# Performance work log

Measured on AMD Instinct MI355X. Metric: run time of the kernel, lower is better.

Reference implementation:

```python
import jax, jax.numpy as jnp
from jax import lax
import numpy as np
import math

B, H, W = 4, 64, 64
D_MODEL, D_STATE, D_CONV, EXPAND, K = 96, 16, 3, 2, 4
D_INNER = EXPAND * D_MODEL          # 192
DT_RANK = math.ceil(D_MODEL / 16)   # 6


def setup_inputs() -> dict:
    key = jax.random.key(0)
    ks = jax.random.split(key, 12)
    s = 0.02
    rgb = jax.random.normal(ks[0], (B, H, W, D_MODEL), jnp.float32)
    t = jax.random.normal(ks[1], (B, H, W, D_MODEL), jnp.float32)
    in_proj1_w = jax.random.normal(ks[2], (2 * D_INNER, D_MODEL), jnp.float32) * s
    in_proj2_w = jax.random.normal(ks[3], (2 * D_INNER, D_MODEL), jnp.float32) * s
    conv1_w = jax.random.normal(ks[4], (D_INNER, 1, D_CONV, D_CONV), jnp.float32) * s
    conv1_b = jnp.zeros((D_INNER,), jnp.float32)
    conv2_w = jax.random.normal(ks[5], (D_INNER, 1, D_CONV, D_CONV), jnp.float32) * s
    conv2_b = jnp.zeros((D_INNER,), jnp.float32)
    x_proj_weight = jax.random.normal(ks[6], (K, DT_RANK + 2 * D_STATE, D_INNER), jnp.float32) * s
    lim = DT_RANK ** -0.5
    dt_projs_weight = jax.random.uniform(ks[7], (K, D_INNER, DT_RANK), jnp.float32, -lim, lim)
    dt = jnp.exp(jax.random.uniform(ks[8], (K, D_INNER), jnp.float32)
                 * (math.log(0.1) - math.log(0.001)) + math.log(0.001))
    dt = jnp.clip(dt, 1e-4, None)
    dt_projs_bias = dt + jnp.log(-jnp.expm1(-dt))  # inverse softplus
    A_logs = jnp.tile(jnp.log(jnp.arange(1, D_STATE + 1, dtype=jnp.float32))[None], (K * D_INNER, 1))
    Ds = jnp.ones((K * D_INNER,), jnp.float32)
    norm1_w = jnp.ones((D_INNER,), jnp.float32); norm1_b = jnp.zeros((D_INNER,), jnp.float32)
    norm2_w = jnp.ones((D_INNER,), jnp.float32); norm2_b = jnp.zeros((D_INNER,), jnp.float32)
    out_proj1_w = jax.random.normal(ks[9], (D_MODEL, D_INNER), jnp.float32) * s
    out_proj2_w = jax.random.normal(ks[10], (D_MODEL, D_INNER), jnp.float32) * s
    return dict(rgb=rgb, t=t, in_proj1_w=in_proj1_w, in_proj2_w=in_proj2_w,
                conv1_w=conv1_w, conv1_b=conv1_b, conv2_w=conv2_w, conv2_b=conv2_b,
                x_proj_weight=x_proj_weight, dt_projs_weight=dt_projs_weight,
                dt_projs_bias=dt_projs_bias, A_logs=A_logs, Ds=Ds,
                norm1_w=norm1_w, norm1_b=norm1_b, norm2_w=norm2_w, norm2_b=norm2_b,
                out_proj1_w=out_proj1_w, out_proj2_w=out_proj2_w)


def _dwconv(x, w, b):
    # x: (B, C, H, W), depthwise 3x3, padding=1
    y = lax.conv_general_dilated(x, w, (1, 1), 'SAME',
                                 feature_group_count=x.shape[1],
                                 dimension_numbers=('NCHW', 'OIHW', 'NCHW'))
    return y + b[None, :, None, None]


def _ln(x, w, b, eps=1e-5):
    m = x.mean(-1, keepdims=True)
    v = ((x - m) ** 2).mean(-1, keepdims=True)
    return (x - m) / jnp.sqrt(v + eps) * w + b


def _cross_scan(x):
    # x: (B, C, H, W) -> (B, 4, C, L): row-major, col-major, and their reverses
    Bz, C, Hh, Ww = x.shape
    L = Hh * Ww
    xr = x.reshape(Bz, C, L)
    xt = x.transpose(0, 1, 3, 2).reshape(Bz, C, L)
    xh = jnp.stack([xr, xt], 1)                        # (B,2,C,L)
    return jnp.concatenate([xh, jnp.flip(xh, -1)], 1)  # (B,4,C,L)


def _cross_merge(y, Hh, Ww):
    # y: (B, 4, C, L) -> (B, C, L); undo scan directions then sum
    Bz, _, C, L = y.shape
    inv = jnp.flip(y[:, 2:4], -1)                      # (B,2,C,L)
    wh = y[:, 1].reshape(Bz, C, Ww, Hh).transpose(0, 1, 3, 2).reshape(Bz, C, L)
    invwh = inv[:, 1].reshape(Bz, C, Ww, Hh).transpose(0, 1, 3, 2).reshape(Bz, C, L)
    return y[:, 0] + inv[:, 0] + wh + invwh


def _selective_scan(u, delta, A, Bs, Cs, Ds, delta_bias):
    # u, delta: (B, K, C, L2); A: (K, C, N); Bs, Cs: (B, K, N, L2); Ds: (K, C)
    Bz, Kk, C, L2 = u.shape
    N = A.shape[-1]
    delta = jax.nn.softplus(delta + delta_bias[None, :, :, None])

    def step(h, inp):
        d_l, u_l, B_l, C_l = inp               # (B,K,C),(B,K,C),(B,K,N),(B,K,N)
        dA = jnp.exp(d_l[..., None] * A[None])            # (B,K,C,N)
        dBu = (d_l * u_l)[..., None] * B_l[:, :, None, :]  # (B,K,C,N)
        h = h * dA + dBu
        y = jnp.einsum('bkcn,bkn->bkc', h, C_l)
        return h, y

    h0 = jnp.zeros((Bz, Kk, C, N), u.dtype)
    seq = (delta.transpose(3, 0, 1, 2), u.transpose(3, 0, 1, 2),
           Bs.transpose(3, 0, 1, 2), Cs.transpose(3, 0, 1, 2))
    _, ys = lax.scan(step, h0, seq)            # (L2, B, K, C)
    y = ys.transpose(1, 2, 3, 0)               # (B, K, C, L2)
    return y + u * Ds[None, :, :, None]


def _forward_core(x1, x2, x_proj_weight, dt_projs_weight, dt_projs_bias, A_logs, Ds):
    # x1, x2: (B, C, H, W)
    Bz, C, Hh, Ww = x1.shape
    L = Hh * Ww
    rgb4 = _cross_scan(x1)                     # (B,4,C,L)
    t4 = _cross_scan(x2)
    # interleave modalities along sequence: [..., rgb_i, t_i, ...] length 2L
    xs = jnp.stack([rgb4, t4], -1).reshape(Bz, K, C, 2 * L)
    x_dbl = jnp.einsum('bkdl,kcd->bkcl', xs, x_proj_weight)
    dts, Bm, Cm = jnp.split(x_dbl, [DT_RANK, DT_RANK + D_STATE], axis=2)
    dts = jnp.einsum('bkrl,kdr->bkdl', dts, dt_projs_weight)   # (B,K,C,2L)
    As = -jnp.exp(A_logs.astype(jnp.float32)).reshape(K, C, D_STATE)
    y = _selective_scan(xs, dts, As, Bm, Cm, Ds.reshape(K, C), dt_projs_bias)
    y = y.reshape(Bz, K, C, L, 2)
    y_rgb = _cross_merge(y[..., 0], Hh, Ww)    # (B,C,L)
    y_t = _cross_merge(y[..., 1], Hh, Ww)
    return y_rgb, y_t


def reference(rgb, t, in_proj1_w, in_proj2_w, conv1_w, conv1_b, conv2_w, conv2_b,
              x_proj_weight, dt_projs_weight, dt_projs_bias, A_logs, Ds,
              norm1_w, norm1_b, norm2_w, norm2_b, out_proj1_w, out_proj2_w):
    Bz, Hh, Ww, _ = rgb.shape
    x1, z1 = jnp.split(rgb @ in_proj1_w.T, 2, -1)
    x2, z2 = jnp.split(t @ in_proj2_w.T, 2, -1)
    x1 = jax.nn.silu(_dwconv(x1.transpose(0, 3, 1, 2), conv1_w, conv1_b))
    x2 = jax.nn.silu(_dwconv(x2.transpose(0, 3, 1, 2), conv2_w, conv2_b))
    y_rgb, y_t = _forward_core(x1, x2, x_proj_weight, dt_projs_weight,
                               dt_projs_bias, A_logs, Ds)
    y_rgb = _ln(y_rgb.transpose(0, 2, 1).reshape(Bz, Hh, Ww, D_INNER), norm1_w, norm1_b)
    y_t = _ln(y_t.transpose(0, 2, 1).reshape(Bz, Hh, Ww, D_INNER), norm2_w, norm2_b)
    out1 = (y_rgb * jax.nn.silu(z1)) @ out_proj1_w.T
    out2 = (y_t * jax.nn.silu(z2)) @ out_proj2_w.T
    return out1, out2
```

## Files before the change

### kernel.cpp

```cpp
#include <hip/hip_runtime.h>
#include <math.h>

#define BB   4
#define LL   4096
#define L2T  8192
#define DM   96
#define CI   192
#define KD   4
#define NN   16
#define RR   6
#define BKT  16
#define SS   128
#define TT   64
#define DBLS 40

#define OFF_XPRE1 0
#define OFF_XPRE2 3145728
#define OFF_Z1    6291456
#define OFF_Z2    9437184
#define OFF_X1C   12582912
#define OFF_X2C   15728640
#define OFF_DBL   18874368
#define OFF_MERG  24117248
#define OFF_DSUM  30408704

__global__ __launch_bounds__(256)
void k_inproj(const float* __restrict__ rgb, const float* __restrict__ tin,
              const float* __restrict__ w1, const float* __restrict__ w2,
              float* __restrict__ xp1, float* __restrict__ xp2,
              float* __restrict__ zz1, float* __restrict__ zz2) {
  int mb = blockIdx.x;
  int nb = blockIdx.y;
  int m  = blockIdx.z;
  const float* in = m ? tin : rgb;
  const float* w  = (m ? w2 : w1) + nb * 96 * DM;
  __shared__ float As[64][100];
  __shared__ float Ws[96][98];
  int t = threadIdx.x;
  const float4* asrc = (const float4*)(in + (size_t)mb * 64 * DM);
  for (int i = t; i < 1536; i += 256) {
    int r = i / 24, kk = (i % 24) * 4;
    *(float4*)&As[r][kk] = asrc[i];
  }
  const float2* wsrc = (const float2*)w;
  for (int i = t; i < 4608; i += 256) {
    int r = i / 48, kk = (i % 48) * 2;
    *(float2*)&Ws[r][kk] = wsrc[i];
  }
  __syncthreads();
  int tc = t & 15, tr = t >> 4;
  float acc[4][6] = {};
  for (int k = 0; k < 96; k += 2) {
    float2 a[4], b[6];
#pragma unroll
    for (int i = 0; i < 4; i++) a[i] = *(const float2*)&As[tr * 4 + i][k];
#pragma unroll
    for (int j = 0; j < 6; j++) b[j] = *(const float2*)&Ws[tc * 6 + j][k];
#pragma unroll
    for (int i = 0; i < 4; i++)
#pragma unroll
      for (int j = 0; j < 6; j++) {
        acc[i][j] = fmaf(a[i].x, b[j].x, acc[i][j]);
        acc[i][j] = fmaf(a[i].y, b[j].y, acc[i][j]);
      }
  }
  float* dst = (nb < 2) ? (m ? xp2 : xp1) : (m ? zz2 : zz1);
  int colbase = (nb & 1) * 96 + tc * 6;
#pragma unroll
  for (int i = 0; i < 4; i++) {
    size_t bl = (size_t)mb * 64 + tr * 4 + i;
#pragma unroll
    for (int j = 0; j < 6; j++)
      dst[bl * CI + colbase + j] = acc[i][j];
  }
}

__global__ __launch_bounds__(256)
void k_conv(const float* __restrict__ xp1, const float* __restrict__ xp2,
            const float* __restrict__ c1w, const float* __restrict__ c1b,
            const float* __restrict__ c2w, const float* __restrict__ c2b,
            float* __restrict__ o1, float* __restrict__ o2) {
  int m = blockIdx.y;
  const float* in = m ? xp2 : xp1;
  const float* cw = m ? c2w : c1w;
  const float* cb = m ? c2b : c1b;
  float* out = m ? o2 : o1;
  int idx = blockIdx.x * 256 + threadIdx.x;
  int c = idx % CI;
  int bl = idx / CI;
  int b = bl / LL, l = bl % LL;
  int hh = l >> 6, ww = l & 63;
  float a = cb[c];
#pragma unroll
  for (int di = 0; di < 3; di++) {
    int h2 = hh + di - 1;
    if ((unsigned)h2 >= 64u) continue;
#pragma unroll
    for (int dj = 0; dj < 3; dj++) {
      int w2 = ww + dj - 1;
      if ((unsigned)w2 >= 64u) continue;
      a = fmaf(in[(b * LL + h2 * 64 + w2) * CI + c], cw[c * 9 + di * 3 + dj], a);
    }
  }
  out[idx] = a / (1.f + __expf(-a));
}

__global__ __launch_bounds__(256)
void k_dbl(const float* __restrict__ x1c, const float* __restrict__ x2c,
           const float* __restrict__ wx, float* __restrict__ dbl) {
  int pt = blockIdx.x;
  int bk = blockIdx.y;
  int b = bk >> 2, k = bk & 3;
  __shared__ float As[64][100];
  __shared__ float Ws[40][100];
  int t = threadIdx.x;
  int tc = t & 7, tr = t >> 3;
  float acc[2][5] = {};
  for (int kc = 0; kc < 2; kc++) {
    if (kc) __syncthreads();
    for (int i = t; i < 1536; i += 256) {
      int r = i / 24, kk = (i % 24) * 4;
      int l2 = pt * 64 + r;
      int mm = l2 & 1, l = l2 >> 1;
      int lt = (k >= 2) ? (LL - 1 - l) : l;
      int sp = (k & 1) ? (((lt & 63) << 6) | (lt >> 6)) : lt;
      const float* src = (mm ? x2c : x1c) + ((size_t)(b * LL + sp)) * CI + kc * 96;
      *(float4*)&As[r][kk] = *(const float4*)(src + kk);
    }
    for (int i = t; i < 960; i += 256) {
      int r = i / 24, kk = (i % 24) * 4;
      float4 v;
      if (r < 38) v = *(const float4*)&wx[(size_t)(k * 38 + r) * CI + kc * 96 + kk];
      else        v = float4{0.f, 0.f, 0.f, 0.f};
      *(float4*)&Ws[r][kk] = v;
    }
    __syncthreads();
    for (int kk2 = 0; kk2 < 96; kk2 += 2) {
      float2 a[2], bv[5];
#pragma unroll
      for (int i = 0; i < 2; i++) a[i] = *(const float2*)&As[tr * 2 + i][kk2];
#pragma unroll
      for (int j = 0; j < 5; j++) bv[j] = *(const float2*)&Ws[tc * 5 + j][kk2];
#pragma unroll
      for (int i = 0; i < 2; i++)
#pragma unroll
        for (int j = 0; j < 5; j++) {
          acc[i][j] = fmaf(a[i].x, bv[j].x, acc[i][j]);
          acc[i][j] = fmaf(a[i].y, bv[j].y, acc[i][j]);
        }
    }
  }
#pragma unroll
  for (int i = 0; i < 2; i++) {
    size_t row = (size_t)bk * L2T + pt * 64 + tr * 2 + i;
#pragma unroll
    for (int j = 0; j < 5; j++) {
      int cc = tc * 5 + j;
      if (cc < 38) dbl[row * DBLS + cc] = acc[i][j];
    }
  }
}

template<int PASS>
__global__ __launch_bounds__(192)
void k_scan(const float* __restrict__ x1c, const float* __restrict__ x2c,
            const float* __restrict__ dbl,
            const float* __restrict__ dtw, const float* __restrict__ dtb,
            const float* __restrict__ alogs, const float* __restrict__ dsv,
            float* __restrict__ hend, float* __restrict__ dsum,
            const float* __restrict__ hin, float* __restrict__ merged) {
  int bid = blockIdx.x;
  int s  = bid & (SS - 1);
  int bk = bid >> 7;
  int b = bk >> 2, kdir = bk & 3;
  int c = threadIdx.x;
  int kc = kdir * CI + c;

  float w2r0 = dtw[kc * RR + 0], w2r1 = dtw[kc * RR + 1], w2r2 = dtw[kc * RR + 2];
  float w2r3 = dtw[kc * RR + 3], w2r4 = dtw[kc * RR + 4], w2r5 = dtw[kc * RR + 5];
  float bias = dtb[kc];
  float Dv   = (PASS == 2) ? dsv[kc] : 0.f;
  float Areg[NN];
#pragma unroll
  for (int n = 0; n < NN; n++) Areg[n] = -__expf(alogs[kc * NN + n]);
  float A1 = Areg[0];
  int ok = 1;
#pragma unroll
  for (int n = 1; n < NN; n++) {
    float want = A1 * (float)(n + 1);
    if (!(fabsf(Areg[n] - want) <= fabsf(want) * 1e-3f + 1e-6f)) ok = 0;
  }
  const bool structured = (__all(ok) != 0);

  float h[NN];
  if (PASS == 2) {
    int base = ((s * BKT + bk) * CI + c) * NN;
#pragma unroll
    for (int n = 0; n < NN; n++) h[n] = hin[base + n];
  } else {
#pragma unroll
    for (int n = 0; n < NN; n++) h[n] = 0.f;
  }
  float dacc = 0.f;

  const float4* dp4 = (const float4*)(dbl + (size_t)(bk * L2T + s * TT) * DBLS);
  const float* u1b = x1c + (size_t)b * LL * CI + c;
  const float* u2b = x2c + (size_t)b * LL * CI + c;

  auto spmap = [&](int l) -> int {
    int lt = (kdir >= 2) ? (LL - 1 - l) : l;
    return (kdir & 1) ? (((lt & 63) << 6) | (lt >> 6)) : lt;
  };

  auto loadrow = [&](float4* Q, int t) {
    const float4* r4 = dp4 + t * 10;
    Q[0] = r4[0]; Q[1] = r4[1]; Q[2] = r4[2];
    Q[3] = r4[3]; Q[4] = r4[4]; Q[5] = r4[5];
    if (PASS == 2) { Q[6] = r4[6]; Q[7] = r4[7]; Q[8] = r4[8]; Q[9] = r4[9]; }
  };

#define DG(Q, i) ((i & 3) == 0 ? Q[(i) >> 2].x : (i & 3) == 1 ? Q[(i) >> 2].y : (i & 3) == 2 ? Q[(i) >> 2].z : Q[(i) >> 2].w)

  auto step = [&](const float4* Q, float u, float& y) {
    float x = bias;
    x = fmaf(DG(Q, 0), w2r0, x); x = fmaf(DG(Q, 1), w2r1, x); x = fmaf(DG(Q, 2), w2r2, x);
    x = fmaf(DG(Q, 3), w2r3, x); x = fmaf(DG(Q, 4), w2r4, x); x = fmaf(DG(Q, 5), w2r5, x);
    float delta = (x > 15.f) ? x : __logf(1.f + __expf(x));
    float du = delta * u;
    float y0 = 0.f, y1 = 0.f, y2 = 0.f, y3 = 0.f;
    if (structured) {
      float r  = __expf(delta * A1);
      float r2 = r * r, r3 = r2 * r, r4 = r2 * r2;
      float r6 = r4 * r2, r8 = r4 * r4;
      float pw[NN];
      pw[0] = r;       pw[1] = r2;      pw[2] = r3;      pw[3] = r4;
      pw[4] = r4 * r;  pw[5] = r6;      pw[6] = r4 * r3; pw[7] = r8;
      pw[8] = r8 * r;  pw[9] = r8 * r2; pw[10] = r8 * r3; pw[11] = r8 * r4;
      pw[12] = r8 * pw[4]; pw[13] = r8 * r6; pw[14] = r8 * pw[6]; pw[15] = r8 * r8;
#pragma unroll
      for (int n = 0; n < NN; n++) {
        h[n] = fmaf(h[n], pw[n], du * DG(Q, 6 + n));
        if (PASS == 2) {
          float* yp = (n & 2) ? ((n & 1) ? &y3 : &y2) : ((n & 1) ? &y1 : &y0);
          *yp = fmaf(h[n], DG(Q, 22 + n), *yp);
        }
      }
    } else {
#pragma unroll
      for (int n = 0; n < NN; n++) {
        float dA = __expf(delta * Areg[n]);
        h[n] = fmaf(h[n], dA, du * DG(Q, 6 + n));
        if (PASS == 2) {
          float* yp = (n & 2) ? ((n & 1) ? &y3 : &y2) : ((n & 1) ? &y1 : &y0);
          *yp = fmaf(h[n], DG(Q, 22 + n), *yp);
        }
      }
    }
    if (PASS == 1) dacc += delta;
    else y = fmaf(u, Dv, (y0 + y1) + (y2 + y3));
  };

  const int NP = TT / 2;
  int l0 = (s * TT) >> 1;
  float4 qA[10], qB[10];
  int spC = spmap(l0);
  float u1C = u1b[(size_t)spC * CI];
  float u2C = u2b[(size_t)spC * CI];
  int spN = spmap(l0 + 1);
  float u1N = u1b[(size_t)spN * CI];
  float u2N = u2b[(size_t)spN * CI];
  int spN2 = spmap(l0 + 2);
  float u1N2 = u1b[(size_t)spN2 * CI];
  float u2N2 = u2b[(size_t)spN2 * CI];
  loadrow(qA, 0);
#pragma unroll 1
  for (int t = 0; t < TT; t += 2) {
    int p = t >> 1;
    loadrow(qB, t + 1);
    int spN3 = 0; float u1N3 = 0.f, u2N3 = 0.f;
    if (p + 3 < NP) {
      spN3 = spmap(l0 + p + 3);
      u1N3 = u1b[(size_t)spN3 * CI];
      u2N3 = u2b[(size_t)spN3 * CI];
    }
    float ya, yb;
    step(qA, u1C, ya);
    if (t + 2 < TT) loadrow(qA, t + 2);
    step(qB, u2C, yb);
    if (PASS == 2) {
      float* mrow = merged + (size_t)(b * LL + spC) * (2 * CI) + c;
      atomicAdd(mrow, ya);
      atomicAdd(mrow + CI, yb);
    }
    spC = spN;  u1C = u1N;  u2C = u2N;
    spN = spN2; u1N = u1N2; u2N = u2N2;
    spN2 = spN3; u1N2 = u1N3; u2N2 = u2N3;
  }
#undef DG

  if (PASS == 1) {
    int base = ((s * BKT + bk) * CI + c) * NN;
#pragma unroll
    for (int n = 0; n < NN; n++) hend[base + n] = h[n];
    dsum[(s * BKT + bk) * CI + c] = dacc;
  }
}

__global__ __launch_bounds__(256)
void k_prop(const float* __restrict__ hend, const float* __restrict__ dsum,
            const float* __restrict__ alogs, float* __restrict__ hin) {
  int idx = blockIdx.x * 256 + threadIdx.x;
  int n = idx & 15;
  int rest = idx >> 4;
  int c = rest % CI;
  int bk = rest / CI;
  int k = bk & 3;
  float A = -__expf(alogs[(k * CI + c) * NN + n]);
  float h = 0.f;
  for (int s = 0; s < SS; s++) {
    int cell = (s * BKT + bk) * CI + c;
    hin[cell * NN + n] = h;
    float ap = __expf(A * dsum[cell]);
    h = h * ap + hend[cell * NN + n];
  }
}

__global__ __launch_bounds__(192)
void k_lngate(float* __restrict__ merged,
              const float* __restrict__ z1, const float* __restrict__ z2,
              const float* __restrict__ n1w, const float* __restrict__ n1b,
              const float* __restrict__ n2w, const float* __restrict__ n2b) {
  int bid = blockIdx.x;
  int m = bid & 1;
  int bl = bid >> 1;
  int c = threadIdx.x;
  float v = merged[(size_t)bid * CI + c];
  float s1 = v, s2 = v * v;
  for (int o = 32; o > 0; o >>= 1) {
    s1 += __shfl_xor(s1, o);
    s2 += __shfl_xor(s2, o);
  }
  __shared__ float red[2][3];
  int wv = threadIdx.x >> 6, ln = threadIdx.x & 63;
  if (ln == 0) { red[0][wv] = s1; red[1][wv] = s2; }
  __syncthreads();
  float S1 = red[0][0] + red[0][1] + red[0][2];
  float S2 = red[1][0] + red[1][1] + red[1][2];
  float mean = S1 * (1.f / CI);
  float var = S2 * (1.f / CI) - mean * mean;
  float rstd = rsqrtf(var + 1e-5f);
  const float* nw = m ? n2w : n1w;
  const float* nb = m ? n2b : n1b;
  float vn = (v - mean) * rstd * nw[c] + nb[c];
  float z = (m ? z2 : z1)[(size_t)bl * CI + c];
  float g = vn * (z / (1.f + __expf(-z)));
  merged[(size_t)bid * CI + c] = g;
}

__global__ __launch_bounds__(256)
void k_outproj(const float* __restrict__ g,
               const float* __restrict__ w1, const float* __restrict__ w2,
               float* __restrict__ out) {
  int mb = blockIdx.x;
  int m  = blockIdx.y;
  const float* w = m ? w2 : w1;
  __shared__ float As[64][100];
  __shared__ float Ws[96][98];
  int t = threadIdx.x;
  int tc = t & 15, tr = t >> 4;
  float acc[4][6] = {};
  for (int kc = 0; kc < 2; kc++) {
    if (kc) __syncthreads();
    for (int i = t; i < 1536; i += 256) {
      int r = i / 24, kk = (i % 24) * 4;
      *(float4*)&As[r][kk] =
          *(const float4*)&g[((size_t)(mb * 64 + r) * 2 + m) * CI + kc * 96 + kk];
    }
    for (int i = t; i < 4608; i += 256) {
      int r = i / 48, kk = (i % 48) * 2;
      *(float2*)&Ws[r][kk] = *(const float2*)&w[(size_t)r * CI + kc * 96 + kk];
    }
    __syncthreads();
    for (int k = 0; k < 96; k += 2) {
      float2 a[4], b[6];
#pragma unroll
      for (int i = 0; i < 4; i++) a[i] = *(const float2*)&As[tr * 4 + i][k];
#pragma unroll
      for (int j = 0; j < 6; j++) b[j] = *(const float2*)&Ws[tc * 6 + j][k];
#pragma unroll
      for (int i = 0; i < 4; i++)
#pragma unroll
        for (int j = 0; j < 6; j++) {
          acc[i][j] = fmaf(a[i].x, b[j].x, acc[i][j]);
          acc[i][j] = fmaf(a[i].y, b[j].y, acc[i][j]);
        }
    }
  }
  float* outp = out + (size_t)m * (BB * LL * DM);
#pragma unroll
  for (int i = 0; i < 4; i++) {
    size_t bl = (size_t)mb * 64 + tr * 4 + i;
#pragma unroll
    for (int j = 0; j < 6; j++)
      outp[bl * DM + tc * 6 + j] = acc[i][j];
  }
}

extern "C" void kernel_launch(void* const* d_in, const int* in_sizes, int n_in,
                              void* d_out, int out_size, void* d_ws, size_t ws_size,
                              hipStream_t stream) {
  const float* rgb = (const float*)d_in[0];
  const float* tin = (const float*)d_in[1];
  const float* ip1 = (const float*)d_in[2];
  const float* ip2 = (const float*)d_in[3];
  const float* c1w = (const float*)d_in[4];
  const float* c1b = (const float*)d_in[5];
  const float* c2w = (const float*)d_in[6];
  const float* c2b = (const float*)d_in[7];
  const float* wx  = (const float*)d_in[8];
  const float* dtw = (const float*)d_in[9];
  const float* dtb = (const float*)d_in[10];
  const float* alg = (const float*)d_in[11];
  const float* Dsp = (const float*)d_in[12];
  const float* n1w = (const float*)d_in[13];
  const float* n1b = (const float*)d_in[14];
  const float* n2w = (const float*)d_in[15];
  const float* n2b = (const float*)d_in[16];
  const float* op1 = (const float*)d_in[17];
  const float* op2 = (const float*)d_in[18];

  float* ws = (float*)d_ws;
  float* xp1 = ws + OFF_XPRE1;
  float* xp2 = ws + OFF_XPRE2;
  float* z1  = ws + OFF_Z1;
  float* z2  = ws + OFF_Z2;
  float* x1c = ws + OFF_X1C;
  float* x2c = ws + OFF_X2C;
  float* dbl = ws + OFF_DBL;
  float* mg  = ws + OFF_MERG;
  float* dsm = ws + OFF_DSUM;
  float* he  = ws + OFF_MERG;
  float* hi  = ws + OFF_XPRE1;
  float* out = (float*)d_out;

  k_inproj<<<dim3(256, 4, 2), 256, 0, stream>>>(rgb, tin, ip1, ip2, xp1, xp2, z1, z2);
  k_conv<<<dim3(12288, 2), 256, 0, stream>>>(xp1, xp2, c1w, c1b, c2w, c2b, x1c, x2c);
  k_dbl<<<dim3(128, 16), 256, 0, stream>>>(x1c, x2c, wx, dbl);
  k_scan<1><<<SS * BKT, 192, 0, stream>>>(x1c, x2c, dbl, dtw, dtb, alg, Dsp, he, dsm, hi, mg);
  k_prop<<<192, 256, 0, stream>>>(he, dsm, alg, hi);
  hipMemsetAsync(mg, 0, (size_t)6291456 * sizeof(float), stream);
  k_scan<2><<<SS * BKT, 192, 0, stream>>>(x1c, x2c, dbl, dtw, dtb, alg, Dsp, he, dsm, hi, mg);
  k_lngate<<<BB * LL * 2, 192, 0, stream>>>(mg, z1, z2, n1w, n1b, n2w, n2b);
  k_outproj<<<dim3(256, 2), 256, 0, stream>>>(mg, op1, op2, out);
}
```

Before: 428.7 us.

## Stage scan dbl rows through double-buffered shared memory chunks

Before, every thread loaded the per-timestep dbl row (dt, B, C) from global memory into registers, even though all 192 threads in a block read the same row. The new code has 160 threads cooperatively copy 16-row chunks into a double-buffered LDS array, prefetching the next chunk in a register while the current one is consumed. Each thread then reads the row by LDS broadcast. This cuts redundant global and L1 traffic and register pressure, at the cost of block-wide __syncthreads per chunk and LDS read latency inside the serial scan loop.

After: 418.9 us. -2.3%, faster.

```diff
diff --git a/kernel.cpp b/kernel.cpp
--- a/kernel.cpp
+++ b/kernel.cpp
@@ -13,6 +13,8 @@
 #define SS   128
 #define TT   64
 #define DBLS 40
+#define CHS  16
+#define NCH  (TT / CHS)
 
 #define OFF_XPRE1 0
 #define OFF_XPRE2 3145728
@@ -169,6 +171,7 @@
             const float* __restrict__ alogs, const float* __restrict__ dsv,
             float* __restrict__ hend, float* __restrict__ dsum,
             const float* __restrict__ hin, float* __restrict__ merged) {
+  __shared__ float sd[2][CHS * DBLS];
   int bid = blockIdx.x;
   int s  = bid & (SS - 1);
   int bk = bid >> 7;
@@ -203,7 +206,7 @@
   }
   float dacc = 0.f;
 
-  const float4* dp4 = (const float4*)(dbl + (size_t)(bk * L2T + s * TT) * DBLS);
+  const float* dpf = dbl + (size_t)(bk * L2T + s * TT) * DBLS;
   const float* u1b = x1c + (size_t)b * LL * CI + c;
   const float* u2b = x2c + (size_t)b * LL * CI + c;
 
@@ -212,11 +215,14 @@
     return (kdir & 1) ? (((lt & 63) << 6) | (lt >> 6)) : lt;
   };
 
-  auto loadrow = [&](float4* Q, int t) {
-    const float4* r4 = dp4 + t * 10;
-    Q[0] = r4[0]; Q[1] = r4[1]; Q[2] = r4[2];
-    Q[3] = r4[3]; Q[4] = r4[4]; Q[5] = r4[5];
-    if (PASS == 2) { Q[6] = r4[6]; Q[7] = r4[7]; Q[8] = r4[8]; Q[9] = r4[9]; }
+  auto ldchunk = [&](int ch) -> float4 {
+    if (threadIdx.x < 160)
+      return *(const float4*)(dpf + ch * (CHS * DBLS) + threadIdx.x * 4);
+    return float4{0.f, 0.f, 0.f, 0.f};
+  };
+  auto wrchunk = [&](int bufi, float4 v) {
+    if (threadIdx.x < 160)
+      *(float4*)&sd[bufi][threadIdx.x * 4] = v;
   };
 
 #define DG(Q, i) ((i & 3) == 0 ? Q[(i) >> 2].x : (i & 3) == 1 ? Q[(i) >> 2].y : (i & 3) == 2 ? Q[(i) >> 2].z : Q[(i) >> 2].w)
@@ -262,7 +268,6 @@
 
   const int NP = TT / 2;
   int l0 = (s * TT) >> 1;
-  float4 qA[10], qB[10];
   int spC = spmap(l0);
   float u1C = u1b[(size_t)spC * CI];
   float u2C = u2b[(size_t)spC * CI];
@@ -272,29 +277,42 @@
   int spN2 = spmap(l0 + 2);
   float u1N2 = u1b[(size_t)spN2 * CI];
   float u2N2 = u2b[(size_t)spN2 * CI];
-  loadrow(qA, 0);
+  float4 stg = ldchunk(0);
+  wrchunk(0, stg);
+  stg = ldchunk(1);
+  __syncthreads();
+
 #pragma unroll 1
-  for (int t = 0; t < TT; t += 2) {
-    int p = t >> 1;
-    loadrow(qB, t + 1);
-    int spN3 = 0; float u1N3 = 0.f, u2N3 = 0.f;
-    if (p + 3 < NP) {
-      spN3 = spmap(l0 + p + 3);
-      u1N3 = u1b[(size_t)spN3 * CI];
-      u2N3 = u2b[(size_t)spN3 * CI];
-    }
-    float ya, yb;
-    step(qA, u1C, ya);
-    if (t + 2 < TT) loadrow(qA, t + 2);
-    step(qB, u2C, yb);
-    if (PASS == 2) {
-      float* mrow = merged + (size_t)(b * LL + spC) * (2 * CI) + c;
-      atomicAdd(mrow, ya);
-      atomicAdd(mrow + CI, yb);
-    }
-    spC = spN;  u1C = u1N;  u2C = u2N;
-    spN = spN2; u1N = u1N2; u2N = u2N2;
-    spN2 = spN3; u1N2 = u1N3; u2N2 = u2N3;
+  for (int ch = 0; ch < NCH; ch++) {
+    const float* cb = sd[ch & 1];
+#pragma unroll 1
+    for (int pp = 0; pp < CHS / 2; pp++) {
+      int p = (ch * CHS) / 2 + pp;
+      const float4* qA = (const float4*)&cb[(pp * 2) * DBLS];
+      const float4* qB = (const float4*)&cb[(pp * 2 + 1) * DBLS];
+      int spN3 = 0; float u1N3 = 0.f, u2N3 = 0.f;
+      if (p + 3 < NP) {
+        spN3 = spmap(l0 + p + 3);
+        u1N3 = u1b[(size_t)spN3 * CI];
+        u2N3 = u2b[(size_t)spN3 * CI];
+      }
+      float ya, yb;
+      step(qA, u1C, ya);
+      step(qB, u2C, yb);
+      if (PASS == 2) {
+        float* mrow = merged + (size_t)(b * LL + spC) * (2 * CI) + c;
+        atomicAdd(mrow, ya);
+        atomicAdd(mrow + CI, yb);
+      }
+      spC = spN;  u1C = u1N;  u2C = u2N;
+      spN = spN2; u1N = u1N2; u2N = u2N2;
+      spN2 = spN3; u1N2 = u1N3; u2N2 = u2N3;
+    }
+    if (ch + 1 < NCH) {
+      wrchunk((ch + 1) & 1, stg);
+      if (ch + 2 < NCH) stg = ldchunk(ch + 2);
+      __syncthreads();
+    }
   }
 #undef DG
 
```
